# Optimization experiments

Measured on AMD Instinct MI355X. Metric: run time of the kernel, lower is better.

Reference implementation:

```python
import jax, jax.numpy as jnp
import numpy as np

B, N, DIM, H, DH, PD = 2, 1024, 768, 8, 64, 4
EPS = 1e-8


def setup_inputs() -> dict:
    key = jax.random.key(0)
    ks = jax.random.split(key, 12)
    w = lambda k, shp: jax.random.normal(k, shp, dtype=jnp.float32) * 0.02
    return {
        "x": jax.random.normal(ks[0], (B, N, DIM), dtype=jnp.float32),
        "rotations": jax.random.normal(ks[1], (B, N, 3, 3), dtype=jnp.float32),
        "translations": jax.random.normal(ks[2], (B, N, 3), dtype=jnp.float32),
        "W_sq": w(ks[3], (H * DH, DIM)),
        "W_sk": w(ks[4], (H * DH, DIM)),
        "W_sv": w(ks[5], (H * DH, DIM)),
        "W_pq": w(ks[6], (H * PD * 3, DIM)),
        "W_pk": w(ks[7], (H * PD * 3, DIM)),
        "W_pv": w(ks[8], (H * PD * 3, DIM)),
        "point_weights": jax.random.normal(ks[9], (H,), dtype=jnp.float32),
        "W_out": w(ks[10], (DIM, H * (DH + PD * 4))),
        "b_out": jax.random.normal(ks[11], (DIM,), dtype=jnp.float32) * 0.02,
    }


def reference(x, rotations, translations, W_sq, W_sk, W_sv, W_pq, W_pk, W_pv, point_weights, W_out, b_out):
    b, n, _ = x.shape
    h, dh, pd = H, DH, PD
    scalar_scale = (2 * dh) ** -0.5           # num_attn_logits=2
    point_scale = (2 * pd * (9 / 2)) ** -0.5

    # scalar q/k/v: [b,h,n,dh]
    qs = (x @ W_sq.T).reshape(b, n, h, dh).transpose(0, 2, 1, 3)
    ks = (x @ W_sk.T).reshape(b, n, h, dh).transpose(0, 2, 1, 3)
    vs = (x @ W_sv.T).reshape(b, n, h, dh).transpose(0, 2, 1, 3)

    # point q/k/v: [b,h,n,pd,3]
    qp = (x @ W_pq.T).reshape(b, n, h, pd, 3).transpose(0, 2, 1, 3, 4)
    kp = (x @ W_pk.T).reshape(b, n, h, pd, 3).transpose(0, 2, 1, 3, 4)
    vp = (x @ W_pv.T).reshape(b, n, h, pd, 3).transpose(0, 2, 1, 3, 4)

    t = translations[:, None, :, None, :]  # [b,1,n,1,3]
    # global-frame points: p_c = sum_r R[n,c,r] * p[d,r] + t
    qp = jnp.einsum('bncr,bhndr->bhndc', rotations, qp) + t
    kp = jnp.einsum('bncr,bhndr->bhndc', rotations, kp) + t
    vp = jnp.einsum('bncr,bhndr->bhndc', rotations, vp) + t

    # scalar attention logits [b,h,i,j]
    logits = jnp.einsum('bhid,bhjd->bhij', qs, ks) * scalar_scale

    # point distance term: sum_{d,c} (q-k)^2 = |q|^2 + |k|^2 - 2 q.k (no [i,j,d,c] tensor)
    q2 = jnp.sum(qp ** 2, axis=(-1, -2))  # [b,h,i]
    k2 = jnp.sum(kp ** 2, axis=(-1, -2))  # [b,h,j]
    qk = jnp.einsum('bhidc,bhjdc->bhij', qp, kp)
    point_dist = q2[..., :, None] + k2[..., None, :] - 2.0 * qk

    pw = jax.nn.softplus(point_weights)[None, :, None, None]  # [1,h,1,1]
    logits = logits - 0.5 * (point_dist * pw * point_scale)

    attn = jax.nn.softmax(logits, axis=-1)

    rs = jnp.einsum('bhij,bhjd->bhid', attn, vs)          # [b,h,n,dh]
    rp = jnp.einsum('bhij,bhjdc->bhidc', attn, vp)        # [b,h,n,pd,3]
    # back to local frame: R^T (p - t)
    rp = jnp.einsum('bnrc,bhndr->bhndc', rotations, rp - t)
    rn = jnp.sqrt(jnp.sum(rp ** 2, axis=-1) + EPS)        # [b,h,n,pd]

    rs = rs.transpose(0, 2, 1, 3).reshape(b, n, h * dh)
    rp_f = rp.transpose(0, 2, 1, 3, 4).reshape(b, n, h * pd * 3)
    rn = rn.transpose(0, 2, 1, 3).reshape(b, n, h * pd)

    results = jnp.concatenate([rs, rp_f, rn], axis=-1)    # [b,n,640]
    return results @ W_out.T + b_out
```

## Files before the change

kernel.cpp:

```cpp
#include <hip/hip_runtime.h>
#include <hip/hip_bf16.h>
#include <math.h>

#define B_  2
#define N_  1024
#define DIM_ 768
#define H_  8
#define DH_ 64
#define PD_ 4
#define NPROJ 1824
#define NPAD  1920
#define BH_ (B_*H_)
#define FDIM 640

#define OFF_RS   0u
#define OFF_RP   (OFF_RS + (size_t)BH_*N_*DH_)
#define OFF_PRAW (OFF_RP + (size_t)BH_*N_*12)
#define OFF_QA   (OFF_PRAW + (size_t)B_*N_*288)
#define OFF_KA   (OFF_QA + (size_t)BH_*N_*96/2)
#define OFF_VT   (OFF_KA + (size_t)BH_*N_*96/2)
#define OFF_XB   (OFF_VT + (size_t)BH_*80*N_/2)
#define OFF_WB   (OFF_XB + (size_t)B_*N_*DIM_/2)
#define OFF_FB   OFF_XB
#define OFF_WOB  OFF_WB

typedef __attribute__((ext_vector_type(8))) short bf16x8;
typedef __attribute__((ext_vector_type(4))) float f32x4;

__device__ __forceinline__ unsigned short f2bf(float f) {
    __hip_bfloat16 h = __float2bfloat16(f);
    return *reinterpret_cast<unsigned short*>(&h);
}

__device__ __forceinline__ unsigned long long pack4(
    unsigned short a, unsigned short b, unsigned short c, unsigned short d)
{
    return (unsigned long long)a
         | ((unsigned long long)b << 16)
         | ((unsigned long long)c << 32)
         | ((unsigned long long)d << 48);
}

__global__ __launch_bounds__(256) void k_cvt_x(
    const float* __restrict__ x, unsigned short* __restrict__ xb)
{
    int i = blockIdx.x * 256 + threadIdx.x;
    if (i >= (B_*N_*DIM_)/4) return;
    float4 v = reinterpret_cast<const float4*>(x)[i];
    reinterpret_cast<unsigned long long*>(xb)[i] =
        pack4(f2bf(v.x), f2bf(v.y), f2bf(v.z), f2bf(v.w));
}

__global__ __launch_bounds__(256) void k_cvt_w(
    const float* __restrict__ Wsq, const float* __restrict__ Wsk,
    const float* __restrict__ Wsv, const float* __restrict__ Wpq,
    const float* __restrict__ Wpk, const float* __restrict__ Wpv,
    unsigned short* __restrict__ wb)
{
    int i = blockIdx.x * 256 + threadIdx.x;
    if (i >= (NPAD*DIM_)/4) return;
    int row = i / (DIM_/4);
    int c4  = i % (DIM_/4);
    unsigned long long o;
    if (row >= NPROJ) {
        o = 0ull;
    } else {
        const float* W;
        if      (row < 512)  W = Wsq + (size_t)row*DIM_;
        else if (row < 1024) W = Wsk + (size_t)(row-512)*DIM_;
        else if (row < 1536) W = Wsv + (size_t)(row-1024)*DIM_;
        else if (row < 1632) W = Wpq + (size_t)(row-1536)*DIM_;
        else if (row < 1728) W = Wpk + (size_t)(row-1632)*DIM_;
        else                 W = Wpv + (size_t)(row-1728)*DIM_;
        float4 v = reinterpret_cast<const float4*>(W)[c4];
        o = pack4(f2bf(v.x), f2bf(v.y), f2bf(v.z), f2bf(v.w));
    }
    reinterpret_cast<unsigned long long*>(wb)[i] = o;
}

__global__ __launch_bounds__(256) void k_cvt_wout(
    const float* __restrict__ Wout, unsigned short* __restrict__ wob)
{
    int i = blockIdx.x * 256 + threadIdx.x;
    if (i >= (DIM_*FDIM)/4) return;
    float4 v = reinterpret_cast<const float4*>(Wout)[i];
    reinterpret_cast<unsigned long long*>(wob)[i] =
        pack4(f2bf(v.x), f2bf(v.y), f2bf(v.z), f2bf(v.w));
}

__device__ __forceinline__ void load_frags2(
    const unsigned short* __restrict__ A0,
    const unsigned short* __restrict__ B0,
    int koff, int ld, bf16x8 a[2], bf16x8 b[2])
{
    #pragma unroll
    for (int m = 0; m < 2; ++m)
        a[m] = *reinterpret_cast<const bf16x8*>(A0 + (size_t)m*16*ld + koff);
    #pragma unroll
    for (int n = 0; n < 2; ++n)
        b[n] = *reinterpret_cast<const bf16x8*>(B0 + (size_t)n*16*ld + koff);
}

__device__ __forceinline__ void mfma4(
    const bf16x8 a[2], const bf16x8 b[2], f32x4 acc[2][2])
{
    #pragma unroll
    for (int m = 0; m < 2; ++m)
        #pragma unroll
        for (int n = 0; n < 2; ++n)
            acc[m][n] = __builtin_amdgcn_mfma_f32_16x16x32_bf16(
                a[m], b[n], acc[m][n], 0, 0, 0);
}

__global__ __launch_bounds__(64, 4) void k_proj_mfma(
    const unsigned short* __restrict__ xb,
    const unsigned short* __restrict__ wb,
    float* __restrict__ ws)
{
    const int lane = threadIdx.x;
    const int lo = lane & 15;
    const int hi = lane >> 4;
    const int bid = blockIdx.x;
    const int L = (bid & 7)*480 + (bid >> 3);
    const int mt = L / 60;
    const int nt = L % 60;
    const int row0 = mt*32;
    const int col0 = nt*32;

    const unsigned short* A0 = xb + (size_t)(row0 + lo)*DIM_ + hi*8;
    const unsigned short* B0 = wb + (size_t)(col0 + lo)*DIM_ + hi*8;

    f32x4 acc[2][2];
    #pragma unroll
    for (int m = 0; m < 2; ++m)
        #pragma unroll
        for (int n = 0; n < 2; ++n) acc[m][n] = (f32x4){0.f,0.f,0.f,0.f};

    bf16x8 aA[2], bA[2], aB[2], bB[2];
    load_frags2(A0, B0, 0, DIM_, aA, bA);
    #pragma unroll
    for (int kt = 0; kt < 24; kt += 2) {
        if (kt + 1 < 24) load_frags2(A0, B0, (kt+1)*32, DIM_, aB, bB);
        mfma4(aA, bA, acc);
        if (kt + 2 < 24) load_frags2(A0, B0, (kt+2)*32, DIM_, aA, bA);
        mfma4(aB, bB, acc);
    }

    unsigned short* qa = (unsigned short*)(ws + OFF_QA);
    unsigned short* ka = (unsigned short*)(ws + OFF_KA);
    unsigned short* vt = (unsigned short*)(ws + OFF_VT);
    float* praw = ws + OFF_PRAW;
    const float ss = 0.08838834764831845f;

    #pragma unroll
    for (int n = 0; n < 2; ++n) {
        int o = col0 + n*16 + lo;
        if (o >= NPROJ) continue;
        if (o >= 1024 && o < 1536) {
            int oo = o - 1024; int h = oo >> 6, c = oo & 63;
            #pragma unroll
            for (int m = 0; m < 2; ++m) {
                int r0 = row0 + m*16 + hi*4;
                int bb = r0 >> 10, nn0 = r0 & (N_-1);
                unsigned long long pk = pack4(
                    f2bf(acc[m][n][0]), f2bf(acc[m][n][1]),
                    f2bf(acc[m][n][2]), f2bf(acc[m][n][3]));
                *reinterpret_cast<unsigned long long*>(
                    vt + ((size_t)(bb*H_ + h)*80 + c)*N_ + nn0) = pk;
            }
        } else {
            #pragma unroll
            for (int m = 0; m < 2; ++m) {
                #pragma unroll
                for (int j = 0; j < 4; ++j) {
                    int r = row0 + m*16 + hi*4 + j;
                    int bb = r >> 10, nn = r & (N_-1);
                    float v = acc[m][n][j];
                    if (o < 512) {
                        int h = o >> 6, c = o & 63;
                        qa[((size_t)(bb*H_ + h)*N_ + nn)*96 + c] = f2bf(v*ss);
                    } else if (o < 1024) {
                        int oo = o - 512; int h = oo >> 6, c = oo & 63;
                        ka[((size_t)(bb*H_ + h)*N_ + nn)*96 + c] = f2bf(v);
                    } else {
                        praw[(size_t)r*288 + (o - 1536)] = v;
                    }
                }
            }
        }
    }
}

__global__ __launch_bounds__(128) void k_prep(
    const float* __restrict__ rot_g,
    const float* __restrict__ trans_g,
    const float* __restrict__ pw_g,
    float* __restrict__ ws)
{
    __shared__ float R[9], T[3];
    __shared__ float rot[3][8][4][3];
    __shared__ float p2[2][8][4];
    __shared__ float q2t[8], k2t[8], coefs[8];
    const int tid = threadIdx.x;
    const int row = blockIdx.x;
    const int b = row >> 10, n = row & (N_-1);

    if (tid < 9)  R[tid] = rot_g[(size_t)row*9 + tid];
    if (tid >= 9 && tid < 12) T[tid-9] = trans_g[(size_t)row*3 + (tid-9)];
    if (tid >= 16 && tid < 24) {
        float pw = pw_g[tid-16];
        coefs[tid-16] = 0.5f * log1pf(__expf(pw)) * (1.0f/6.0f);
    }
    __syncthreads();
    if (tid < 96) {
        int which = tid >> 5, idx = tid & 31;
        int h = idx >> 2, pd = idx & 3;
        const float* p = ws + OFF_PRAW + (size_t)row*288 + which*96 + h*12 + pd*3;
        float px = p[0], py = p[1], pz = p[2];
        float c0 = R[0]*px + R[1]*py + R[2]*pz + T[0];
        float c1 = R[3]*px + R[4]*py + R[5]*pz + T[1];
        float c2 = R[6]*px + R[7]*py + R[8]*pz + T[2];
        rot[which][h][pd][0] = c0;
        rot[which][h][pd][1] = c1;
        rot[which][h][pd][2] = c2;
        if (which < 2) p2[which][h][pd] = c0*c0 + c1*c1 + c2*c2;
    }
    __syncthreads();
    if (tid < 16) {
        int w = tid >> 3, h = tid & 7;
        float s = p2[w][h][0] + p2[w][h][1] + p2[w][h][2] + p2[w][h][3];
        if (w) k2t[h] = s; else q2t[h] = s;
    }
    __syncthreads();

    unsigned short* qa = (unsigned short*)(ws + OFF_QA);
    unsigned short* ka = (unsigned short*)(ws + OFF_KA);
    unsigned short* vt = (unsigned short*)(ws + OFF_VT);

    for (int i = tid; i < 256; i += 128) {
        int h = i >> 5, c = i & 31;
        float qv, kv;
        if (c < 12)      { qv = rot[0][h][c/3][c%3] * 2.f * coefs[h]; kv = rot[1][h][c/3][c%3]; }
        else if (c == 12){ qv = q2t[h];  kv = -coefs[h]; }
        else if (c == 13){ qv = 1.f;     kv = -coefs[h]*k2t[h]; }
        else             { qv = 0.f;     kv = 0.f; }
        size_t base = ((size_t)(b*H_ + h)*N_ + n)*96 + 64 + c;
        qa[base] = f2bf(qv);
        ka[base] = f2bf(kv);
    }
    {
        int h = tid >> 4, r = tid & 15;
        float vv = (r < 12) ? rot[2][h][r/3][r%3] : 0.f;
        vt[((size_t)(b*H_ + h)*80 + 64 + r)*N_ + n] = f2bf(vv);
    }
}

#define VPAD 72
#define APAD 84
__global__ __launch_bounds__(512, 4) void k_attn_mfma(
    const unsigned short* __restrict__ qa_g,
    const unsigned short* __restrict__ ka_g,
    const unsigned short* __restrict__ vt_g,
    float* __restrict__ ws)
{
    __shared__ unsigned short sP[8][16*VPAD];
    __shared__ float sAcc[3][2][16][APAD];
    __shared__ float sML[3][2][16][2];

    const int tid  = threadIdx.x;
    const int lane = tid & 63;
    const int wid  = tid >> 6;
    const int lo = lane & 15;
    const int hi = lane >> 4;
    const int bid = blockIdx.x;
    const int Lb = (bid & 7)*64 + (bid >> 3);
    const int bh = Lb >> 5;
    const int qt = Lb & 31;
    const int q0 = qt * 32;
    const int qh = wid & 1;
    const int kq = wid >> 1;
    const int mrow = qh * 16;

    const unsigned short* Qa = qa_g + (size_t)bh*N_*96;
    const unsigned short* Ka = ka_g + (size_t)bh*N_*96;
    const unsigned short* Vt = vt_g + (size_t)bh*80*N_;

    bf16x8 qfr[3];
    {
        int qrow = q0 + mrow + lo;
        #pragma unroll
        for (int c = 0; c < 3; ++c)
            qfr[c] = *reinterpret_cast<const bf16x8*>(
                Qa + (size_t)qrow*96 + c*32 + hi*8);
    }

    f32x4 acc[5];
    #pragma unroll
    for (int d = 0; d < 5; ++d) acc[d] = (f32x4){0.f,0.f,0.f,0.f};
    float m[4] = {-1e30f,-1e30f,-1e30f,-1e30f};
    float l[4] = {0.f,0.f,0.f,0.f};

    for (int it = 0; it < 4; ++it) {
        const int j0 = (kq*4 + it)*64;

        bf16x8 kb[3][4];
        #pragma unroll
        for (int c = 0; c < 3; ++c)
            #pragma unroll
            for (int t = 0; t < 4; ++t)
                kb[c][t] = *reinterpret_cast<const bf16x8*>(
                    Ka + (size_t)(j0 + t*16 + lo)*96 + c*32 + hi*8);

        f32x4 s[4];
        #pragma unroll
        for (int t = 0; t < 4; ++t) s[t] = (f32x4){0.f,0.f,0.f,0.f};
        #pragma unroll
        for (int c = 0; c < 3; ++c)
            #pragma unroll
            for (int t = 0; t < 4; ++t)
                s[t] = __builtin_amdgcn_mfma_f32_16x16x32_bf16(qfr[c], kb[c][t], s[t], 0, 0, 0);

        bf16x8 vb[2][5];
        #pragma unroll
        for (int kk = 0; kk < 2; ++kk)
            #pragma unroll
            for (int dt = 0; dt < 5; ++dt)
                vb[kk][dt] = *reinterpret_cast<const bf16x8*>(
                    Vt + (size_t)(dt*16 + lo)*N_ + j0 + kk*32 + hi*8);

        float scl[4];
        #pragma unroll
        for (int r = 0; r < 4; ++r) {
            float v = fmaxf(fmaxf(s[0][r], s[1][r]), fmaxf(s[2][r], s[3][r]));
            v = fmaxf(v, __shfl_xor(v, 1));
            v = fmaxf(v, __shfl_xor(v, 2));
            v = fmaxf(v, __shfl_xor(v, 4));
            v = fmaxf(v, __shfl_xor(v, 8));
            float mn = fmaxf(m[r], v);
            scl[r] = __expf(m[r] - mn);
            m[r] = mn;
        }
        float ps[4] = {0.f,0.f,0.f,0.f};
        #pragma unroll
        for (int t = 0; t < 4; ++t) {
            #pragma unroll
            for (int r = 0; r < 4; ++r) {
                float p = __expf(s[t][r] - m[r]);
                ps[r] += p;
                sP[wid][(hi*4 + r)*VPAD + t*16 + lo] = f2bf(p);
            }
        }
        #pragma unroll
        for (int r = 0; r < 4; ++r) {
            float v = ps[r];
            v += __shfl_xor(v, 1);
            v += __shfl_xor(v, 2);
            v += __shfl_xor(v, 4);
            v += __shfl_xor(v, 8);
            l[r] = l[r]*scl[r] + v;
        }
        #pragma unroll
        for (int d = 0; d < 5; ++d)
            #pragma unroll
            for (int r = 0; r < 4; ++r) acc[d][r] *= scl[r];

        #pragma unroll
        for (int kk = 0; kk < 2; ++kk) {
            bf16x8 pa = *reinterpret_cast<const bf16x8*>(
                &sP[wid][lo*VPAD + kk*32 + hi*8]);
            #pragma unroll
            for (int dt = 0; dt < 5; ++dt)
                acc[dt] = __builtin_amdgcn_mfma_f32_16x16x32_bf16(pa, vb[kk][dt], acc[dt], 0, 0, 0);
        }
    }

    if (kq > 0) {
        #pragma unroll
        for (int r = 0; r < 4; ++r) {
            int rl = hi*4 + r;
            #pragma unroll
            for (int dt = 0; dt < 5; ++dt)
                sAcc[kq-1][qh][rl][dt*16 + lo] = acc[dt][r];
            if (lo == 0) { sML[kq-1][qh][rl][0] = m[r]; sML[kq-1][qh][rl][1] = l[r]; }
        }
    }
    __syncthreads();
    if (kq == 0) {
        float* ws_rs = ws + OFF_RS + (size_t)bh*N_*DH_;
        float* ws_rp = ws + OFF_RP + (size_t)bh*N_*12;
        #pragma unroll
        for (int r = 0; r < 4; ++r) {
            int rl = hi*4 + r;
            float mp[3], lp[3];
            float mm = m[r];
            #pragma unroll
            for (int p = 0; p < 3; ++p) {
                mp[p] = sML[p][qh][rl][0];
                lp[p] = sML[p][qh][rl][1];
                mm = fmaxf(mm, mp[p]);
            }
            float f0 = __expf(m[r] - mm);
            float Lsum = l[r]*f0;
            float fp[3];
            #pragma unroll
            for (int p = 0; p < 3; ++p) {
                fp[p] = __expf(mp[p] - mm);
                Lsum += lp[p]*fp[p];
            }
            float inv = 1.f / Lsum;
            int i = q0 + mrow + rl;
            #pragma unroll
            for (int dt = 0; dt < 5; ++dt) {
                float val = acc[dt][r]*f0;
                #pragma unroll
                for (int p = 0; p < 3; ++p)
                    val += sAcc[p][qh][rl][dt*16 + lo]*fp[p];
                val *= inv;
                int d = dt*16 + lo;
                if (d < 64)
                    ws_rs[(size_t)i*DH_ + d] = val;
                else if (d - 64 < 12)
                    ws_rp[(size_t)i*12 + (d - 64)] = val;
            }
        }
    }
}

__global__ __launch_bounds__(256) void k_fin_prep(
    const float* __restrict__ rotations,
    const float* __restrict__ translations,
    const float* __restrict__ ws,
    unsigned short* __restrict__ fb)
{
    __shared__ float sF[8][FDIM];
    const int tid = threadIdx.x;
    const int row0 = blockIdx.x * 8;
    const int b = row0 >> 10;
    const float* ws_rs = ws + OFF_RS;
    const float* ws_rp = ws + OFF_RP;

    for (int i = tid; i < 8*512; i += 256) {
        int r = i >> 9, f = i & 511;
        int h = f >> 6, c = f & 63;
        int n = (row0 & (N_-1)) + r;
        sF[r][f] = ws_rs[(((size_t)(b*H_ + h))*N_ + n)*DH_ + c];
    }
    {
        int r = tid >> 5;
        int idx = tid & 31;
        int h = idx >> 2, pd = idx & 3;
        int row = row0 + r;
        int n = row & (N_-1);
        const float* rp = ws_rp + (((size_t)(b*H_ + h))*N_ + n)*12 + pd*3;
        const float* R = rotations + (size_t)row*9;
        const float* T = translations + (size_t)row*3;
        float d0 = rp[0] - T[0], d1 = rp[1] - T[1], d2 = rp[2] - T[2];
        float l0 = R[0]*d0 + R[3]*d1 + R[6]*d2;
        float l1 = R[1]*d0 + R[4]*d1 + R[7]*d2;
        float l2 = R[2]*d0 + R[5]*d1 + R[8]*d2;
        sF[r][512 + h*12 + pd*3 + 0] = l0;
        sF[r][512 + h*12 + pd*3 + 1] = l1;
        sF[r][512 + h*12 + pd*3 + 2] = l2;
        sF[r][608 + h*4 + pd] = sqrtf(l0*l0 + l1*l1 + l2*l2 + 1e-8f);
    }
    __syncthreads();

    #pragma unroll
    for (int r = 0; r < 8; ++r) {
        for (int f4 = tid; f4 < FDIM/4; f4 += 256) {
            unsigned long long pk = pack4(
                f2bf(sF[r][f4*4+0]), f2bf(sF[r][f4*4+1]),
                f2bf(sF[r][f4*4+2]), f2bf(sF[r][f4*4+3]));
            reinterpret_cast<unsigned long long*>(fb + (size_t)(row0 + r)*FDIM)[f4] = pk;
        }
    }
}

__global__ __launch_bounds__(64, 4) void k_out_mfma(
    const unsigned short* __restrict__ fb,
    const unsigned short* __restrict__ wob,
    const float* __restrict__ bout,
    float* __restrict__ out)
{
    const int lane = threadIdx.x;
    const int lo = lane & 15;
    const int hi = lane >> 4;
    const int bid = blockIdx.x;
    const int L = (bid & 7)*192 + (bid >> 3);
    const int mt = L / 24;
    const int nt = L % 24;
    const int row0 = mt*32;
    const int col0 = nt*32;

    const unsigned short* A0 = fb  + (size_t)(row0 + lo)*FDIM + hi*8;
    const unsigned short* B0 = wob + (size_t)(col0 + lo)*FDIM + hi*8;

    f32x4 acc[2][2];
    #pragma unroll
    for (int m = 0; m < 2; ++m)
        #pragma unroll
        for (int n = 0; n < 2; ++n) acc[m][n] = (f32x4){0.f,0.f,0.f,0.f};

    bf16x8 aA[2], bA[2], aB[2], bB[2];
    load_frags2(A0, B0, 0, FDIM, aA, bA);
    #pragma unroll
    for (int kt = 0; kt < 20; kt += 2) {
        if (kt + 1 < 20) load_frags2(A0, B0, (kt+1)*32, FDIM, aB, bB);
        mfma4(aA, bA, acc);
        if (kt + 2 < 20) load_frags2(A0, B0, (kt+2)*32, FDIM, aA, bA);
        mfma4(aB, bB, acc);
    }

    #pragma unroll
    for (int n = 0; n < 2; ++n) {
        int o = col0 + n*16 + lo;
        float bo = bout[o];
        #pragma unroll
        for (int m = 0; m < 2; ++m) {
            #pragma unroll
            for (int j = 0; j < 4; ++j) {
                int r = row0 + m*16 + hi*4 + j;
                out[(size_t)r*DIM_ + o] = acc[m][n][j] + bo;
            }
        }
    }
}

extern "C" void kernel_launch(void* const* d_in, const int* in_sizes, int n_in,
                              void* d_out, int out_size, void* d_ws, size_t ws_size,
                              hipStream_t stream) {
    const float* x            = (const float*)d_in[0];
    const float* rotations    = (const float*)d_in[1];
    const float* translations = (const float*)d_in[2];
    const float* Wsq          = (const float*)d_in[3];
    const float* Wsk          = (const float*)d_in[4];
    const float* Wsv          = (const float*)d_in[5];
    const float* Wpq          = (const float*)d_in[6];
    const float* Wpk          = (const float*)d_in[7];
    const float* Wpv          = (const float*)d_in[8];
    const float* pweights     = (const float*)d_in[9];
    const float* Wout         = (const float*)d_in[10];
    const float* bout         = (const float*)d_in[11];
    float* out = (float*)d_out;
    float* ws  = (float*)d_ws;

    unsigned short* xb  = (unsigned short*)(ws + OFF_XB);
    unsigned short* wb  = (unsigned short*)(ws + OFF_WB);
    unsigned short* qa  = (unsigned short*)(ws + OFF_QA);
    unsigned short* ka  = (unsigned short*)(ws + OFF_KA);
    unsigned short* vt  = (unsigned short*)(ws + OFF_VT);
    unsigned short* fb  = (unsigned short*)(ws + OFF_FB);
    unsigned short* wob = (unsigned short*)(ws + OFF_WOB);

    k_cvt_x<<<(B_*N_*DIM_/4 + 255)/256, 256, 0, stream>>>(x, xb);
    k_cvt_w<<<(NPAD*DIM_/4 + 255)/256, 256, 0, stream>>>(Wsq, Wsk, Wsv, Wpq, Wpk, Wpv, wb);
    k_proj_mfma<<<3840, 64, 0, stream>>>(xb, wb, ws);
    k_prep<<<B_*N_, 128, 0, stream>>>(rotations, translations, pweights, ws);
    k_attn_mfma<<<BH_*32, 512, 0, stream>>>(qa, ka, vt, ws);
    k_cvt_wout<<<(DIM_*FDIM/4 + 255)/256, 256, 0, stream>>>(Wout, wob);
    k_fin_prep<<<B_*N_/8, 256, 0, stream>>>(rotations, translations, ws, fb);
    k_out_mfma<<<1536, 64, 0, stream>>>(fb, wob, bout, out);
}
```

Measured before the change: 118.2 us.

## Fuse fp32-to-bf16 conversion into projection and output GEMM loads

```diff
diff --git a/kernel.cpp b/kernel.cpp
--- a/kernel.cpp
+++ b/kernel.cpp
@@ -9,7 +9,6 @@
 #define DH_ 64
 #define PD_ 4
 #define NPROJ 1824
-#define NPAD  1920
 #define BH_ (B_*H_)
 #define FDIM 640
 
@@ -19,10 +18,7 @@
 #define OFF_QA   (OFF_PRAW + (size_t)B_*N_*288)
 #define OFF_KA   (OFF_QA + (size_t)BH_*N_*96/2)
 #define OFF_VT   (OFF_KA + (size_t)BH_*N_*96/2)
-#define OFF_XB   (OFF_VT + (size_t)BH_*80*N_/2)
-#define OFF_WB   (OFF_XB + (size_t)B_*N_*DIM_/2)
-#define OFF_FB   OFF_XB
-#define OFF_WOB  OFF_WB
+#define OFF_FB   (OFF_VT + (size_t)BH_*80*N_/2)
 
 typedef __attribute__((ext_vector_type(8))) short bf16x8;
 typedef __attribute__((ext_vector_type(4))) float f32x4;
@@ -41,94 +37,50 @@
          | ((unsigned long long)d << 48);
 }
 
-__global__ __launch_bounds__(256) void k_cvt_x(
-    const float* __restrict__ x, unsigned short* __restrict__ xb)
-{
-    int i = blockIdx.x * 256 + threadIdx.x;
-    if (i >= (B_*N_*DIM_)/4) return;
-    float4 v = reinterpret_cast<const float4*>(x)[i];
-    reinterpret_cast<unsigned long long*>(xb)[i] =
-        pack4(f2bf(v.x), f2bf(v.y), f2bf(v.z), f2bf(v.w));
-}
-
-__global__ __launch_bounds__(256) void k_cvt_w(
+__device__ __forceinline__ bf16x8 cvt8(const float* __restrict__ p)
+{
+    float4 u = *reinterpret_cast<const float4*>(p);
+    float4 v = *reinterpret_cast<const float4*>(p + 4);
+    bf16x8 r;
+    r[0] = (short)f2bf(u.x); r[1] = (short)f2bf(u.y);
+    r[2] = (short)f2bf(u.z); r[3] = (short)f2bf(u.w);
+    r[4] = (short)f2bf(v.x); r[5] = (short)f2bf(v.y);
+    r[6] = (short)f2bf(v.z); r[7] = (short)f2bf(v.w);
+    return r;
+}
+
+__global__ __launch_bounds__(64, 4) void k_proj_mfma(
+    const float* __restrict__ x,
     const float* __restrict__ Wsq, const float* __restrict__ Wsk,
     const float* __restrict__ Wsv, const float* __restrict__ Wpq,
     const float* __restrict__ Wpk, const float* __restrict__ Wpv,
-    unsigned short* __restrict__ wb)
-{
-    int i = blockIdx.x * 256 + threadIdx.x;
-    if (i >= (NPAD*DIM_)/4) return;
-    int row = i / (DIM_/4);
-    int c4  = i % (DIM_/4);
-    unsigned long long o;
-    if (row >= NPROJ) {
-        o = 0ull;
-    } else {
-        const float* W;
-        if      (row < 512)  W = Wsq + (size_t)row*DIM_;
-        else if (row < 1024) W = Wsk + (size_t)(row-512)*DIM_;
-        else if (row < 1536) W = Wsv + (size_t)(row-1024)*DIM_;
-        else if (row < 1632) W = Wpq + (size_t)(row-1536)*DIM_;
-        else if (row < 1728) W = Wpk + (size_t)(row-1632)*DIM_;
-        else                 W = Wpv + (size_t)(row-1728)*DIM_;
-        float4 v = reinterpret_cast<const float4*>(W)[c4];
-        o = pack4(f2bf(v.x), f2bf(v.y), f2bf(v.z), f2bf(v.w));
-    }
-    reinterpret_cast<unsigned long long*>(wb)[i] = o;
-}
-
-__global__ __launch_bounds__(256) void k_cvt_wout(
-    const float* __restrict__ Wout, unsigned short* __restrict__ wob)
-{
-    int i = blockIdx.x * 256 + threadIdx.x;
-    if (i >= (DIM_*FDIM)/4) return;
-    float4 v = reinterpret_cast<const float4*>(Wout)[i];
-    reinterpret_cast<unsigned long long*>(wob)[i] =
-        pack4(f2bf(v.x), f2bf(v.y), f2bf(v.z), f2bf(v.w));
-}
-
-__device__ __forceinline__ void load_frags2(
-    const unsigned short* __restrict__ A0,
-    const unsigned short* __restrict__ B0,
-    int koff, int ld, bf16x8 a[2], bf16x8 b[2])
-{
-    #pragma unroll
-    for (int m = 0; m < 2; ++m)
-        a[m] = *reinterpret_cast<const bf16x8*>(A0 + (size_t)m*16*ld + koff);
-    #pragma unroll
-    for (int n = 0; n < 2; ++n)
-        b[n] = *reinterpret_cast<const bf16x8*>(B0 + (size_t)n*16*ld + koff);
-}
-
-__device__ __forceinline__ void mfma4(
-    const bf16x8 a[2], const bf16x8 b[2], f32x4 acc[2][2])
-{
-    #pragma unroll
-    for (int m = 0; m < 2; ++m)
-        #pragma unroll
-        for (int n = 0; n < 2; ++n)
-            acc[m][n] = __builtin_amdgcn_mfma_f32_16x16x32_bf16(
-                a[m], b[n], acc[m][n], 0, 0, 0);
-}
-
-__global__ __launch_bounds__(64, 4) void k_proj_mfma(
-    const unsigned short* __restrict__ xb,
-    const unsigned short* __restrict__ wb,
     float* __restrict__ ws)
 {
     const int lane = threadIdx.x;
     const int lo = lane & 15;
     const int hi = lane >> 4;
     const int bid = blockIdx.x;
-    const int L = (bid & 7)*480 + (bid >> 3);
-    const int mt = L / 60;
-    const int nt = L % 60;
+    const int L = (bid & 7)*456 + (bid >> 3);
+    const int mt = L / 57;
+    const int nt = L % 57;
     const int row0 = mt*32;
     const int col0 = nt*32;
 
-    const unsigned short* A0 = xb + (size_t)(row0 + lo)*DIM_ + hi*8;
-    const unsigned short* B0 = wb + (size_t)(col0 + lo)*DIM_ + hi*8;
+    const float* A0 = x + (size_t)(row0 + lo)*DIM_ + hi*8;
+
+    const float* Bp[2];
+    #pragma unroll
+    for (int n = 0; n < 2; ++n) {
+        int o0 = col0 + n*16;
+        const float* W; int base;
+        if      (o0 < 512)  { W = Wsq; base = 0;    }
+        else if (o0 < 1024) { W = Wsk; base = 512;  }
+        else if (o0 < 1536) { W = Wsv; base = 1024; }
+        else if (o0 < 1632) { W = Wpq; base = 1536; }
+        else if (o0 < 1728) { W = Wpk; base = 1632; }
+        else                { W = Wpv; base = 1728; }
+        Bp[n] = W + (size_t)(o0 + lo - base)*DIM_ + hi*8;
+    }
 
     f32x4 acc[2][2];
     #pragma unroll
@@ -136,14 +88,17 @@
         #pragma unroll
         for (int n = 0; n < 2; ++n) acc[m][n] = (f32x4){0.f,0.f,0.f,0.f};
 
-    bf16x8 aA[2], bA[2], aB[2], bB[2];
-    load_frags2(A0, B0, 0, DIM_, aA, bA);
-    #pragma unroll
-    for (int kt = 0; kt < 24; kt += 2) {
-        if (kt + 1 < 24) load_frags2(A0, B0, (kt+1)*32, DIM_, aB, bB);
-        mfma4(aA, bA, acc);
-        if (kt + 2 < 24) load_frags2(A0, B0, (kt+2)*32, DIM_, aA, bA);
-        mfma4(aB, bB, acc);
+    #pragma unroll
+    for (int kt = 0; kt < 24; ++kt) {
+        const int koff = kt*32;
+        bf16x8 a0 = cvt8(A0 + koff);
+        bf16x8 a1 = cvt8(A0 + (size_t)16*DIM_ + koff);
+        bf16x8 b0 = cvt8(Bp[0] + koff);
+        bf16x8 b1 = cvt8(Bp[1] + koff);
+        acc[0][0] = __builtin_amdgcn_mfma_f32_16x16x32_bf16(a0, b0, acc[0][0], 0, 0, 0);
+        acc[0][1] = __builtin_amdgcn_mfma_f32_16x16x32_bf16(a0, b1, acc[0][1], 0, 0, 0);
+        acc[1][0] = __builtin_amdgcn_mfma_f32_16x16x32_bf16(a1, b0, acc[1][0], 0, 0, 0);
+        acc[1][1] = __builtin_amdgcn_mfma_f32_16x16x32_bf16(a1, b1, acc[1][1], 0, 0, 0);
     }
 
     unsigned short* qa = (unsigned short*)(ws + OFF_QA);
@@ -155,7 +110,6 @@
     #pragma unroll
     for (int n = 0; n < 2; ++n) {
         int o = col0 + n*16 + lo;
-        if (o >= NPROJ) continue;
         if (o >= 1024 && o < 1536) {
             int oo = o - 1024; int h = oo >> 6, c = oo & 63;
             #pragma unroll
@@ -478,7 +432,7 @@
 
 __global__ __launch_bounds__(64, 4) void k_out_mfma(
     const unsigned short* __restrict__ fb,
-    const unsigned short* __restrict__ wob,
+    const float* __restrict__ Wout,
     const float* __restrict__ bout,
     float* __restrict__ out)
 {
@@ -492,8 +446,8 @@
     const int row0 = mt*32;
     const int col0 = nt*32;
 
-    const unsigned short* A0 = fb  + (size_t)(row0 + lo)*FDIM + hi*8;
-    const unsigned short* B0 = wob + (size_t)(col0 + lo)*FDIM + hi*8;
+    const unsigned short* A0 = fb + (size_t)(row0 + lo)*FDIM + hi*8;
+    const float* B0 = Wout + (size_t)(col0 + lo)*FDIM + hi*8;
 
     f32x4 acc[2][2];
     #pragma unroll
@@ -501,14 +455,17 @@
         #pragma unroll
         for (int n = 0; n < 2; ++n) acc[m][n] = (f32x4){0.f,0.f,0.f,0.f};
 
-    bf16x8 aA[2], bA[2], aB[2], bB[2];
-    load_frags2(A0, B0, 0, FDIM, aA, bA);
-    #pragma unroll
-    for (int kt = 0; kt < 20; kt += 2) {
-        if (kt + 1 < 20) load_frags2(A0, B0, (kt+1)*32, FDIM, aB, bB);
-        mfma4(aA, bA, acc);
-        if (kt + 2 < 20) load_frags2(A0, B0, (kt+2)*32, FDIM, aA, bA);
-        mfma4(aB, bB, acc);
+    #pragma unroll
+    for (int kt = 0; kt < 20; ++kt) {
+        const int koff = kt*32;
+        bf16x8 a0 = *reinterpret_cast<const bf16x8*>(A0 + koff);
+        bf16x8 a1 = *reinterpret_cast<const bf16x8*>(A0 + (size_t)16*FDIM + koff);
+        bf16x8 b0 = cvt8(B0 + koff);
+        bf16x8 b1 = cvt8(B0 + (size_t)16*FDIM + koff);
+        acc[0][0] = __builtin_amdgcn_mfma_f32_16x16x32_bf16(a0, b0, acc[0][0], 0, 0, 0);
+        acc[0][1] = __builtin_amdgcn_mfma_f32_16x16x32_bf16(a0, b1, acc[0][1], 0, 0, 0);
+        acc[1][0] = __builtin_amdgcn_mfma_f32_16x16x32_bf16(a1, b0, acc[1][0], 0, 0, 0);
+        acc[1][1] = __builtin_amdgcn_mfma_f32_16x16x32_bf16(a1, b1, acc[1][1], 0, 0, 0);
     }
 
     #pragma unroll
@@ -544,20 +501,14 @@
     float* out = (float*)d_out;
     float* ws  = (float*)d_ws;
 
-    unsigned short* xb  = (unsigned short*)(ws + OFF_XB);
-    unsigned short* wb  = (unsigned short*)(ws + OFF_WB);
-    unsigned short* qa  = (unsigned short*)(ws + OFF_QA);
-    unsigned short* ka  = (unsigned short*)(ws + OFF_KA);
-    unsigned short* vt  = (unsigned short*)(ws + OFF_VT);
-    unsigned short* fb  = (unsigned short*)(ws + OFF_FB);
-    unsigned short* wob = (unsigned short*)(ws + OFF_WOB);
-
-    k_cvt_x<<<(B_*N_*DIM_/4 + 255)/256, 256, 0, stream>>>(x, xb);
-    k_cvt_w<<<(NPAD*DIM_/4 + 255)/256, 256, 0, stream>>>(Wsq, Wsk, Wsv, Wpq, Wpk, Wpv, wb);
-    k_proj_mfma<<<3840, 64, 0, stream>>>(xb, wb, ws);
+    unsigned short* qa = (unsigned short*)(ws + OFF_QA);
+    unsigned short* ka = (unsigned short*)(ws + OFF_KA);
+    unsigned short* vt = (unsigned short*)(ws + OFF_VT);
+    unsigned short* fb = (unsigned short*)(ws + OFF_FB);
+
+    k_proj_mfma<<<3648, 64, 0, stream>>>(x, Wsq, Wsk, Wsv, Wpq, Wpk, Wpv, ws);
     k_prep<<<B_*N_, 128, 0, stream>>>(rotations, translations, pweights, ws);
     k_attn_mfma<<<BH_*32, 512, 0, stream>>>(qa, ka, vt, ws);
-    k_cvt_wout<<<(DIM_*FDIM/4 + 255)/256, 256, 0, stream>>>(Wout, wob);
     k_fin_prep<<<B_*N_/8, 256, 0, stream>>>(rotations, translations, ws, fb);
-    k_out_mfma<<<1536, 64, 0, stream>>>(fb, wob, bout, out);
-}
+    k_out_mfma<<<1536, 64, 0, stream>>>(fb, Wout, bout, out);
+}
```

After: 152.7 us. 29.2% more time.
